# Optimization experiments

Measured on AMD Instinct MI355X. Metric: run time of the kernel, lower is better.

The kernel has to match this reference:

```python
import jax, jax.numpy as jnp
import numpy as np

B, T, E = 2, 2048, 2048
H, HKV, D = 32, 8, 64
G = H // HKV  # groups = 4
ROPE_BASE = 10000.0


def setup_inputs() -> dict:
    key = jax.random.key(0)
    ks = jax.random.split(key, 5)
    s = 0.02
    return {
        "x": jax.random.normal(ks[0], (B, T, E), dtype=jnp.float32),
        "Wq": jax.random.normal(ks[1], (E, H * D), dtype=jnp.float32) * s,
        "Wk": jax.random.normal(ks[2], (E, HKV * D), dtype=jnp.float32) * s,
        "Wv": jax.random.normal(ks[3], (E, HKV * D), dtype=jnp.float32) * s,
        "Wo": jax.random.normal(ks[4], (E, E), dtype=jnp.float32) * s,
    }


def _rope_tables(t, d, dtype):
    # standard rotate-half RoPE, theta base 10000
    inv_freq = 1.0 / (ROPE_BASE ** (jnp.arange(0, d, 2, dtype=jnp.float32) / d))
    ang = jnp.arange(t, dtype=jnp.float32)[:, None] * inv_freq[None, :]  # [T, D/2]
    return jnp.cos(ang).astype(dtype), jnp.sin(ang).astype(dtype)


def _apply_rope(x, cos, sin):
    # x: [B, h, T, D]; cos/sin: [T, D/2]
    d2 = x.shape[-1] // 2
    x1, x2 = x[..., :d2], x[..., d2:]
    return jnp.concatenate([x1 * cos - x2 * sin, x2 * cos + x1 * sin], axis=-1)


def reference(x, Wq, Wk, Wv, Wo):
    b, t, _ = x.shape
    q = (x @ Wq).reshape(b, t, H, D).transpose(0, 2, 1, 3)      # [B,H,T,D]
    k = (x @ Wk).reshape(b, t, HKV, D).transpose(0, 2, 1, 3)    # [B,HKV,T,D]
    v = (x @ Wv).reshape(b, t, HKV, D).transpose(0, 2, 1, 3)    # [B,HKV,T,D]

    cos, sin = _rope_tables(t, D, x.dtype)
    q = _apply_rope(q, cos, sin)
    k = _apply_rope(k, cos, sin)

    # GQA: keep KV unexpanded, broadcast groups inside the contraction
    qg = q.reshape(b, HKV, G, t, D)
    scale = 1.0 / np.sqrt(D)
    scores = jnp.einsum('bkgtd,bksd->bkgts', qg, k) * scale      # [B,HKV,G,T,T]
    causal = jnp.tril(jnp.ones((t, t), dtype=bool))
    scores = jnp.where(causal, scores, jnp.finfo(scores.dtype).min)
    attn = jax.nn.softmax(scores, axis=-1)
    y = jnp.einsum('bkgts,bksd->bkgtd', attn, v)                 # [B,HKV,G,T,D]
    y = y.reshape(b, H, t, D).transpose(0, 2, 1, 3).reshape(b, t, H * D)
    return y @ Wo
```

## Files before the change

kernel.cpp:

```cpp
#include <hip/hip_runtime.h>
#include <hip/hip_bf16.h>
#include <cstdint>
#include <cstddef>

typedef __bf16 bf16;
typedef __attribute__((ext_vector_type(8))) __bf16 bf16x8;
typedef __attribute__((ext_vector_type(4))) __bf16 bf16x4v;
typedef __attribute__((ext_vector_type(4))) float f32x4;

#define NB 2
#define NT 2048
#define NE 2048
#define NH 32
#define NHKV 8
#define ND 64
#define NBT (NB * NT)
#define NQKV 3072

__device__ __forceinline__ void gload_lds16(const void* g, void* l) {
  __builtin_amdgcn_global_load_lds(
      (const __attribute__((address_space(1))) unsigned int*)g,
      (__attribute__((address_space(3))) unsigned int*)l, 16, 0, 0);
}

__device__ __forceinline__ int swz(int row, int byteoff) {
  return (row * 128 + byteoff) ^ ((row & 7) << 4);
}


__global__ void cvt_bf16_kernel(const float* __restrict__ in, bf16* __restrict__ out, int n4) {
  int i = blockIdx.x * blockDim.x + threadIdx.x;
  const int stride = gridDim.x * blockDim.x;
  for (; i < n4; i += stride) {
    const float4 v = ((const float4*)in)[i];
    bf16x4v o;
    o[0] = (bf16)v.x; o[1] = (bf16)v.y; o[2] = (bf16)v.z; o[3] = (bf16)v.w;
    ((bf16x4v*)out)[i] = o;
  }
}

__global__ void transpose_cvt_kernel(const float* __restrict__ in, bf16* __restrict__ out,
                                     int ncols, int rowoff) {
  __shared__ float tile[32][33];
  const int c0 = blockIdx.x * 32;
  const int k0 = blockIdx.y * 32;
  const int tx = threadIdx.x, ty = threadIdx.y;
#pragma unroll
  for (int j = 0; j < 4; ++j)
    tile[ty + j * 8][tx] = in[(size_t)(k0 + ty + j * 8) * ncols + c0 + tx];
  __syncthreads();
#pragma unroll
  for (int j = 0; j < 4; ++j)
    out[(size_t)(rowoff + c0 + ty + j * 8) * 2048 + k0 + tx] = (bf16)tile[tx][ty + j * 8];
}

__global__ void rope_table_kernel(float* __restrict__ tab) {
  int i = blockIdx.x * 256 + threadIdx.x;
  if (i >= NT * 32) return;
  const int t = i >> 5, d = i & 31;
  const float inv = expf(-(float)d * 0.28782313662425574f);
  const float ang = (float)t * inv;
  tab[t * 64 + d] = cosf(ang);
  tab[t * 64 + 32 + d] = sinf(ang);
}


template <typename CT, bool ROPE>
__global__ __launch_bounds__(256, 3)
void gemm_r3_kernel(const bf16* __restrict__ A, const bf16* __restrict__ Bt,
                    CT* __restrict__ C, int M, int N, int K,
                    const float* __restrict__ tab, bf16* __restrict__ vt) {
  __shared__ __align__(16) bf16 As[3][128 * 32];
  __shared__ __align__(16) bf16 Bs[3][128 * 32];
  const int tid = threadIdx.x;
  const int lane = tid & 63, wid = tid >> 6;
  const int wr = wid >> 1, wc = wid & 1;
  const int cpx = (int)gridDim.x >> 3;
  const int swzb = ((int)blockIdx.x & 7) * cpx + ((int)blockIdx.x >> 3);
  const int gx = N >> 7;
  const int bx = swzb % gx, by = swzb / gx;
  const int m0 = by * 128, n0 = bx * 128;
  const int srow = tid >> 2;
  const int skoff = 8 * ((tid & 3) ^ ((tid >> 3) & 3));
  const bf16* ga = A + (size_t)(m0 + srow) * K + skoff;
  const bf16* gb = Bt + (size_t)(n0 + srow) * K + skoff;
  const int fr = lane & 15;
  const int fq = lane >> 4;
  const int fks = 8 * (fq ^ ((fr >> 1) & 3));
  const int NTK = K >> 5;
  f32x4 acc[4][4] = {};

#define STAGE_T(b, t)                                                   \
  do {                                                                  \
    const int kk = (t) * 32;                                            \
    gload_lds16(ga + kk, &As[b][tid * 8]);                              \
    gload_lds16(ga + kk + (size_t)64 * K, &As[b][2048 + tid * 8]);      \
    gload_lds16(gb + kk, &Bs[b][tid * 8]);                              \
    gload_lds16(gb + kk + (size_t)64 * K, &Bs[b][2048 + tid * 8]);      \
  } while (0)

  STAGE_T(0, 0);
  STAGE_T(1, 1);

  int bc = 0;
  for (int t = 0; t < NTK; ++t) {
    if (t + 1 < NTK) asm volatile("s_waitcnt vmcnt(4)" ::: "memory");
    else             asm volatile("s_waitcnt vmcnt(0)" ::: "memory");
    __builtin_amdgcn_s_barrier();

    bf16x8 af[4], bfr[4];
#pragma unroll
    for (int m = 0; m < 4; ++m)
      af[m] = *(const bf16x8*)&As[bc][(wr * 64 + m * 16 + fr) * 32 + fks];
#pragma unroll
    for (int n = 0; n < 4; ++n)
      bfr[n] = *(const bf16x8*)&Bs[bc][(wc * 64 + n * 16 + fr) * 32 + fks];

    if (t + 2 < NTK) {
      const int pb = (bc + 2 >= 3) ? bc - 1 : bc + 2;
      STAGE_T(pb, t + 2);
    }

    __builtin_amdgcn_s_setprio(1);
#pragma unroll
    for (int m = 0; m < 4; ++m)
#pragma unroll
      for (int n = 0; n < 4; ++n)
        acc[m][n] = __builtin_amdgcn_mfma_f32_16x16x32_bf16(af[m], bfr[n], acc[m][n], 0, 0, 0);
    __builtin_amdgcn_s_setprio(0);
    bc = (bc + 1 == 3) ? 0 : bc + 1;
  }
#undef STAGE_T

  const int colbase = n0 + wc * 64;

  if (ROPE && colbase >= 2560) {
    const int hk = (colbase - 2560) >> 6;
    const int bb = m0 >> 11;
    const int t0 = (m0 & (NT - 1)) + wr * 64 + fq * 4;
    bf16* vtp = vt + (size_t)(bb * NHKV + hk) * 64 * NT;
#pragma unroll
    for (int m = 0; m < 4; ++m) {
#pragma unroll
      for (int n = 0; n < 4; ++n) {
        const int d = n * 16 + fr;
        bf16x4v w;
        w[0] = (bf16)acc[m][n][0];
        w[1] = (bf16)acc[m][n][1];
        w[2] = (bf16)acc[m][n][2];
        w[3] = (bf16)acc[m][n][3];
        *(bf16x4v*)&vtp[(size_t)d * NT + t0 + m * 16] = w;
      }
    }
    return;
  }

  const bool do_rope = ROPE && colbase < 2560;
  const bool do_scale = ROPE && colbase < 2048;
  const float SCALE = 0.18033688011112042f;
  const int orow0 = m0 + wr * 64 + fq * 4;
  const int ocol0 = colbase + fr;
#pragma unroll
  for (int m = 0; m < 4; ++m) {
#pragma unroll
    for (int j = 0; j < 4; ++j) {
      const int row = orow0 + m * 16 + j;
      float v0 = acc[m][0][j], v1 = acc[m][1][j], v2 = acc[m][2][j], v3 = acc[m][3][j];
      if (do_rope) {
        const int tt = row & (NT - 1);
        const float c0 = tab[tt * 64 + fr],      s0 = tab[tt * 64 + 32 + fr];
        const float c1 = tab[tt * 64 + 16 + fr], s1 = tab[tt * 64 + 48 + fr];
        const float a0 = v0, a2 = v2;
        v0 = a0 * c0 - a2 * s0;
        v2 = a2 * c0 + a0 * s0;
        const float a1 = v1, a3 = v3;
        v1 = a1 * c1 - a3 * s1;
        v3 = a3 * c1 + a1 * s1;
        if (do_scale) { v0 *= SCALE; v1 *= SCALE; v2 *= SCALE; v3 *= SCALE; }
      }
      CT* cp = &C[(size_t)row * N + ocol0];
      cp[0] = (CT)v0; cp[16] = (CT)v1; cp[32] = (CT)v2; cp[48] = (CT)v3;
    }
  }
}


__global__ __launch_bounds__(256, 3)
void attn_kernel(const bf16* __restrict__ qkv, const bf16* __restrict__ vt,
                 bf16* __restrict__ y) {
  const int bid = blockIdx.x;
  const int qtb = 15 - (bid >> 6);
  const int bh = bid & 63;
  const int b = bh >> 5, h = bh & 31, hk = h >> 2;
  const int q0 = qtb * 128;

  __shared__ __align__(16) bf16 Kb[3][4096], Vb[3][4096];

  const int tid = threadIdx.x;
  const int lane = tid & 63, wid = tid >> 6;
  const int ql = lane & 15;
  const int sub = lane >> 4;

  const int st_r = tid >> 3;
  const int kperm = 4 * (st_r >> 4) + 8 * ((st_r >> 2) & 3) + (st_r & 3);
  const int csw = ((tid & 7) ^ (st_r & 7)) * 8;
  const bf16* kgbase = qkv + (size_t)(b * NT + kperm) * NQKV + 2048 + hk * 64 + csw;
  const bf16* vgbase = vt + ((size_t)(b * NHKV + hk) * 64 + st_r) * NT + csw;

  auto STAGE = [&](int buf, int kv0) {
    const bf16* kg = kgbase + (size_t)kv0 * NQKV;
    gload_lds16(kg, Kb[buf] + tid * 8);
    gload_lds16(kg + (size_t)32 * NQKV, Kb[buf] + 2048 + tid * 8);
    const bf16* vg = vgbase + kv0;
    gload_lds16(vg, Vb[buf] + tid * 8);
    gload_lds16(vg + 32 * NT, Vb[buf] + 2048 + tid * 8);
  };

  bf16x8 qf[2][2];
#pragma unroll
  for (int set = 0; set < 2; ++set) {
    const bf16* qp = qkv + (size_t)(b * NT + q0 + wid * 32 + set * 16 + ql) * NQKV + h * 64 + sub * 8;
    qf[set][0] = *(const bf16x8*)qp;
    qf[set][1] = *(const bf16x8*)(qp + 32);
  }

  bf16x8 ones8;
#pragma unroll
  for (int i = 0; i < 8; ++i) ones8[i] = (bf16)1.0f;

  f32x4 o[2][4] = {};
  f32x4 ol[2] = {};
  float m_s[2] = {-1e30f, -1e30f};

  const int ntiles = 2 * qtb + 2;
  STAGE(0, 0);
  STAGE(1, 64);

  int bc = 0;
  for (int it = 0; it < ntiles; ++it) {
    const int kv0 = it * 64;
    if (it + 1 < ntiles) asm volatile("s_waitcnt vmcnt(4)" ::: "memory");
    else                 asm volatile("s_waitcnt vmcnt(0)" ::: "memory");
    __builtin_amdgcn_s_barrier();

    if (it + 2 < ntiles) {
      const int pb = (bc + 2 >= 3) ? bc - 1 : bc + 2;
      STAGE(pb, kv0 + 128);
    }

    if (kv0 <= q0 + wid * 32 + 47) {
      bf16x8 kf[4][2];
#pragma unroll
      for (int n = 0; n < 4; ++n)
#pragma unroll
        for (int c = 0; c < 2; ++c)
          kf[n][c] = *(const bf16x8*)((const char*)Kb[bc] + swz(n * 16 + ql, c * 64 + sub * 16));
      bf16x8 vf[2][4];
#pragma unroll
      for (int kc = 0; kc < 2; ++kc)
#pragma unroll
        for (int dt = 0; dt < 4; ++dt)
          vf[kc][dt] = *(const bf16x8*)((const char*)Vb[bc] + swz(dt * 16 + ql, kc * 64 + sub * 16));

#pragma unroll
      for (int set = 0; set < 2; ++set) {
        const int qlo = q0 + wid * 32 + set * 16;
        if (kv0 > qlo + 15) continue;

        f32x4 s[4] = {};
        __builtin_amdgcn_s_setprio(1);
#pragma unroll
        for (int n = 0; n < 4; ++n) {
          s[n] = __builtin_amdgcn_mfma_f32_16x16x32_bf16(kf[n][0], qf[set][0], s[n], 0, 0, 0);
          s[n] = __builtin_amdgcn_mfma_f32_16x16x32_bf16(kf[n][1], qf[set][1], s[n], 0, 0, 0);
        }
        __builtin_amdgcn_s_setprio(0);

        float p[4][4];
        if (kv0 + 63 > qlo) {
          const int qrow = qlo + ql;
#pragma unroll
          for (int n = 0; n < 4; ++n) {
            const int kvb = kv0 + 32 * (n >> 1) + 4 * (n & 1) + 8 * sub;
#pragma unroll
            for (int j = 0; j < 4; ++j)
              p[n][j] = (kvb + j > qrow) ? -1e30f : s[n][j];
          }
        } else {
#pragma unroll
          for (int n = 0; n < 4; ++n)
#pragma unroll
            for (int j = 0; j < 4; ++j)
              p[n][j] = s[n][j];
        }

        float rmax = p[0][0];
#pragma unroll
        for (int n = 0; n < 4; ++n)
#pragma unroll
          for (int j = 0; j < 4; ++j) rmax = fmaxf(rmax, p[n][j]);
        rmax = fmaxf(rmax, __shfl_xor(rmax, 16));
        rmax = fmaxf(rmax, __shfl_xor(rmax, 32));

        if (!__all(rmax <= m_s[set] + 8.0f)) {
          const float mnew = fmaxf(m_s[set], rmax);
          const float sc = exp2f(m_s[set] - mnew);
          m_s[set] = mnew;
          ol[set] *= sc;
#pragma unroll
          for (int dt = 0; dt < 4; ++dt) o[set][dt] *= sc;
        }
        const float mcur = m_s[set];

        bf16x8 pb2[2];
#pragma unroll
        for (int n = 0; n < 4; ++n)
#pragma unroll
          for (int j = 0; j < 4; ++j)
            pb2[n >> 1][(n & 1) * 4 + j] = (bf16)exp2f(p[n][j] - mcur);

        __builtin_amdgcn_s_setprio(1);
#pragma unroll
        for (int kc = 0; kc < 2; ++kc) {
          ol[set] = __builtin_amdgcn_mfma_f32_16x16x32_bf16(ones8, pb2[kc], ol[set], 0, 0, 0);
#pragma unroll
          for (int dt = 0; dt < 4; ++dt)
            o[set][dt] = __builtin_amdgcn_mfma_f32_16x16x32_bf16(vf[kc][dt], pb2[kc], o[set][dt], 0, 0, 0);
        }
        __builtin_amdgcn_s_setprio(0);
      }
    }
    bc = (bc + 1 == 3) ? 0 : bc + 1;
  }

#pragma unroll
  for (int set = 0; set < 2; ++set) {
    const float inv = 1.0f / ol[set][0];
    bf16* yp = y + (size_t)(b * NT + q0 + wid * 32 + set * 16 + ql) * NE + h * 64 + sub * 4;
#pragma unroll
    for (int dt = 0; dt < 4; ++dt) {
      bf16x4v w;
      w[0] = (bf16)(o[set][dt][0] * inv);
      w[1] = (bf16)(o[set][dt][1] * inv);
      w[2] = (bf16)(o[set][dt][2] * inv);
      w[3] = (bf16)(o[set][dt][3] * inv);
      *(bf16x4v*)(yp + dt * 16) = w;
    }
  }
}


extern "C" void kernel_launch(void* const* d_in, const int* in_sizes, int n_in,
                              void* d_out, int out_size, void* d_ws, size_t ws_size,
                              hipStream_t stream) {
  const float* x = (const float*)d_in[0];
  const float* Wq = (const float*)d_in[1];
  const float* Wk = (const float*)d_in[2];
  const float* Wv = (const float*)d_in[3];
  const float* Wo = (const float*)d_in[4];
  float* out = (float*)d_out;

  char* ws = (char*)d_ws;
  size_t off = 0;
  auto alloc = [&](size_t bytes) -> void* {
    void* p = ws + off;
    off += (bytes + 255) & ~(size_t)255;
    return p;
  };
  bf16* xb = (bf16*)alloc((size_t)NBT * NE * 2);
  bf16* wqkv_t = (bf16*)alloc((size_t)NQKV * NE * 2);
  bf16* wo_t = (bf16*)alloc((size_t)NE * NE * 2);
  bf16* qkv = (bf16*)alloc((size_t)NBT * NQKV * 2);
  bf16* vtb = (bf16*)alloc((size_t)NB * NHKV * ND * NT * 2);
  bf16* yb = (bf16*)alloc((size_t)NBT * NE * 2);
  float* tab = (float*)alloc((size_t)NT * 64 * 4);

  cvt_bf16_kernel<<<2048, 256, 0, stream>>>(x, xb, NBT * NE / 4);
  dim3 tb(32, 8);
  transpose_cvt_kernel<<<dim3(64, 64), tb, 0, stream>>>(Wq, wqkv_t, 2048, 0);
  transpose_cvt_kernel<<<dim3(16, 64), tb, 0, stream>>>(Wk, wqkv_t, 512, 2048);
  transpose_cvt_kernel<<<dim3(16, 64), tb, 0, stream>>>(Wv, wqkv_t, 512, 2560);
  transpose_cvt_kernel<<<dim3(64, 64), tb, 0, stream>>>(Wo, wo_t, 2048, 0);
  rope_table_kernel<<<(NT * 32 + 255) / 256, 256, 0, stream>>>(tab);

  gemm_r3_kernel<bf16, true><<<dim3((NQKV / 128) * (NBT / 128)), 256, 0, stream>>>(
      xb, wqkv_t, qkv, NBT, NQKV, NE, tab, vtb);
  attn_kernel<<<dim3(NT / 128 * 64), 256, 0, stream>>>(qkv, vtb, yb);
  gemm_r3_kernel<float, false><<<dim3((NE / 128) * (NBT / 128)), 256, 0, stream>>>(
      yb, wo_t, out, NBT, NE, NE, nullptr, nullptr);
}
```

Baseline: 199.5 us.

## Fuse prep kernels into one launch and double-buffer attention for higher occupancy

Merges the x conversion, the four weight transpose-conversions and the RoPE table kernel into a single prep kernel that dispatches on block index, removing five kernel launches. The attention kernel goes from a three-stage to a two-stage K/V LDS pipeline with launch bounds raised to 5 blocks per CU, trading prefetch depth for occupancy. The row-max reduction is also restructured into a shallower tree. The risk is that the single-tile prefetch with a full vmcnt(0) wait exposes more memory latency per iteration.

```diff
diff --git a/kernel.cpp b/kernel.cpp
--- a/kernel.cpp
+++ b/kernel.cpp
@@ -28,40 +28,51 @@
 }
 
 
-__global__ void cvt_bf16_kernel(const float* __restrict__ in, bf16* __restrict__ out, int n4) {
-  int i = blockIdx.x * blockDim.x + threadIdx.x;
-  const int stride = gridDim.x * blockDim.x;
-  for (; i < n4; i += stride) {
-    const float4 v = ((const float4*)in)[i];
-    bf16x4v o;
-    o[0] = (bf16)v.x; o[1] = (bf16)v.y; o[2] = (bf16)v.z; o[3] = (bf16)v.w;
-    ((bf16x4v*)out)[i] = o;
-  }
-}
-
-__global__ void transpose_cvt_kernel(const float* __restrict__ in, bf16* __restrict__ out,
-                                     int ncols, int rowoff) {
+__global__ __launch_bounds__(256)
+void prep_kernel(const float* __restrict__ x, const float* __restrict__ Wq,
+                 const float* __restrict__ Wk, const float* __restrict__ Wv,
+                 const float* __restrict__ Wo, bf16* __restrict__ xb,
+                 bf16* __restrict__ wqkv_t, bf16* __restrict__ wo_t,
+                 float* __restrict__ tab) {
+  const int bid = blockIdx.x, tid = threadIdx.x;
+
+  if (bid < 1024) {
+    const int n4 = NBT * NE / 4;
+    for (int i = bid * 256 + tid; i < n4; i += 1024 * 256) {
+      const float4 v = ((const float4*)x)[i];
+      bf16x4v o;
+      o[0] = (bf16)v.x; o[1] = (bf16)v.y; o[2] = (bf16)v.z; o[3] = (bf16)v.w;
+      ((bf16x4v*)xb)[i] = o;
+    }
+    return;
+  }
+  if (bid < 1280) {
+    const int i = (bid - 1024) * 256 + tid;
+    const int t = i >> 5, d = i & 31;
+    const float inv = expf(-(float)d * 0.28782313662425574f);
+    const float ang = (float)t * inv;
+    tab[t * 64 + d] = cosf(ang);
+    tab[t * 64 + 32 + d] = sinf(ang);
+    return;
+  }
+
   __shared__ float tile[32][33];
-  const int c0 = blockIdx.x * 32;
-  const int k0 = blockIdx.y * 32;
-  const int tx = threadIdx.x, ty = threadIdx.y;
+  const float* in;
+  bf16* outp;
+  int ncols, rowoff, gx, sub;
+  if (bid < 5376)      { sub = bid - 1280; in = Wq; outp = wqkv_t; ncols = 2048; rowoff = 0;    gx = 64; }
+  else if (bid < 6400) { sub = bid - 5376; in = Wk; outp = wqkv_t; ncols = 512;  rowoff = 2048; gx = 16; }
+  else if (bid < 7424) { sub = bid - 6400; in = Wv; outp = wqkv_t; ncols = 512;  rowoff = 2560; gx = 16; }
+  else                 { sub = bid - 7424; in = Wo; outp = wo_t;   ncols = 2048; rowoff = 0;    gx = 64; }
+  const int c0 = (sub % gx) * 32, k0 = (sub / gx) * 32;
+  const int tx = tid & 31, ty = tid >> 5;
 #pragma unroll
   for (int j = 0; j < 4; ++j)
     tile[ty + j * 8][tx] = in[(size_t)(k0 + ty + j * 8) * ncols + c0 + tx];
   __syncthreads();
 #pragma unroll
   for (int j = 0; j < 4; ++j)
-    out[(size_t)(rowoff + c0 + ty + j * 8) * 2048 + k0 + tx] = (bf16)tile[tx][ty + j * 8];
-}
-
-__global__ void rope_table_kernel(float* __restrict__ tab) {
-  int i = blockIdx.x * 256 + threadIdx.x;
-  if (i >= NT * 32) return;
-  const int t = i >> 5, d = i & 31;
-  const float inv = expf(-(float)d * 0.28782313662425574f);
-  const float ang = (float)t * inv;
-  tab[t * 64 + d] = cosf(ang);
-  tab[t * 64 + 32 + d] = sinf(ang);
+    outp[(size_t)(rowoff + c0 + ty + j * 8) * 2048 + k0 + tx] = (bf16)tile[tx][ty + j * 8];
 }
 
 
@@ -185,7 +196,7 @@
 }
 
 
-__global__ __launch_bounds__(256, 3)
+__global__ __launch_bounds__(256, 5)
 void attn_kernel(const bf16* __restrict__ qkv, const bf16* __restrict__ vt,
                  bf16* __restrict__ y) {
   const int bid = blockIdx.x;
@@ -194,7 +205,7 @@
   const int b = bh >> 5, h = bh & 31, hk = h >> 2;
   const int q0 = qtb * 128;
 
-  __shared__ __align__(16) bf16 Kb[3][4096], Vb[3][4096];
+  __shared__ __align__(16) bf16 Kb[2][4096], Vb[2][4096];
 
   const int tid = threadIdx.x;
   const int lane = tid & 63, wid = tid >> 6;
@@ -234,19 +245,13 @@
 
   const int ntiles = 2 * qtb + 2;
   STAGE(0, 0);
-  STAGE(1, 64);
-
-  int bc = 0;
+
   for (int it = 0; it < ntiles; ++it) {
     const int kv0 = it * 64;
-    if (it + 1 < ntiles) asm volatile("s_waitcnt vmcnt(4)" ::: "memory");
-    else                 asm volatile("s_waitcnt vmcnt(0)" ::: "memory");
+    const int bc = it & 1;
+    asm volatile("s_waitcnt vmcnt(0)" ::: "memory");
     __builtin_amdgcn_s_barrier();
-
-    if (it + 2 < ntiles) {
-      const int pb = (bc + 2 >= 3) ? bc - 1 : bc + 2;
-      STAGE(pb, kv0 + 128);
-    }
+    if (it + 1 < ntiles) STAGE(bc ^ 1, kv0 + 64);
 
     if (kv0 <= q0 + wid * 32 + 47) {
       bf16x8 kf[4][2];
@@ -294,11 +299,12 @@
               p[n][j] = s[n][j];
         }
 
-        float rmax = p[0][0];
-#pragma unroll
-        for (int n = 0; n < 4; ++n)
-#pragma unroll
-          for (int j = 0; j < 4; ++j) rmax = fmaxf(rmax, p[n][j]);
+        const float r0 = fmaxf(fmaxf(p[0][0], p[0][1]), p[0][2]);
+        const float r1 = fmaxf(fmaxf(p[0][3], p[1][0]), p[1][1]);
+        const float r2 = fmaxf(fmaxf(p[1][2], p[1][3]), p[2][0]);
+        const float r3 = fmaxf(fmaxf(p[2][1], p[2][2]), p[2][3]);
+        const float r4 = fmaxf(fmaxf(p[3][0], p[3][1]), p[3][2]);
+        float rmax = fmaxf(fmaxf(fmaxf(r0, r1), r2), fmaxf(fmaxf(r3, r4), p[3][3]));
         rmax = fmaxf(rmax, __shfl_xor(rmax, 16));
         rmax = fmaxf(rmax, __shfl_xor(rmax, 32));
 
@@ -330,7 +336,6 @@
         __builtin_amdgcn_s_setprio(0);
       }
     }
-    bc = (bc + 1 == 3) ? 0 : bc + 1;
   }
 
 #pragma unroll
@@ -375,14 +380,7 @@
   bf16* yb = (bf16*)alloc((size_t)NBT * NE * 2);
   float* tab = (float*)alloc((size_t)NT * 64 * 4);
 
-  cvt_bf16_kernel<<<2048, 256, 0, stream>>>(x, xb, NBT * NE / 4);
-  dim3 tb(32, 8);
-  transpose_cvt_kernel<<<dim3(64, 64), tb, 0, stream>>>(Wq, wqkv_t, 2048, 0);
-  transpose_cvt_kernel<<<dim3(16, 64), tb, 0, stream>>>(Wk, wqkv_t, 512, 2048);
-  transpose_cvt_kernel<<<dim3(16, 64), tb, 0, stream>>>(Wv, wqkv_t, 512, 2560);
-  transpose_cvt_kernel<<<dim3(64, 64), tb, 0, stream>>>(Wo, wo_t, 2048, 0);
-  rope_table_kernel<<<(NT * 32 + 255) / 256, 256, 0, stream>>>(tab);
-
+  prep_kernel<<<11520, 256, 0, stream>>>(x, Wq, Wk, Wv, Wo, xb, wqkv_t, wo_t, tab);
   gemm_r3_kernel<bf16, true><<<dim3((NQKV / 128) * (NBT / 128)), 256, 0, stream>>>(
       xb, wqkv_t, qkv, NBT, NQKV, NE, tab, vtb);
   attn_kernel<<<dim3(NT / 128 * 64), 256, 0, stream>>>(qkv, vtb, yb);
```

New measurement: 562.3 us. 182% more time.
